# Optimization experiments

Measured on AMD Instinct MI355X. Metric: run time of the kernel, lower is better.

Reference implementation:

```python
import jax, jax.numpy as jnp
import numpy as np

B, N, D = 4, 2048, 1024
HEADS, DIM_HEAD = 16, 64
INNER = HEADS * DIM_HEAD  # 1024
SCALE = DIM_HEAD ** -0.5


def setup_inputs() -> dict:
    key = jax.random.key(0)
    ks = jax.random.split(key, 8)
    w = 0.02
    return {
        "x":  jax.random.normal(ks[0], (B, N, D), dtype=jnp.float32),
        "Wq": jax.random.normal(ks[1], (D, INNER), dtype=jnp.float32) * w,
        "bq": jax.random.normal(ks[2], (INNER,), dtype=jnp.float32) * w,
        "Wv": jax.random.normal(ks[3], (D, INNER), dtype=jnp.float32) * w,
        "bv": jax.random.normal(ks[4], (INNER,), dtype=jnp.float32) * w,
        "Wo": jax.random.normal(ks[5], (INNER, D), dtype=jnp.float32) * w,
        "bo": jax.random.normal(ks[6], (D,), dtype=jnp.float32) * w,
    }


def reference(x, Wq, bq, Wv, bv, Wo, bo):
    b, n, _ = x.shape
    q = x @ Wq + bq                      # [b, n, inner]
    v = x @ Wv + bv                      # [b, n, inner]
    # split heads -> [b, h, n, d]
    q = q.reshape(b, n, HEADS, DIM_HEAD).transpose(0, 2, 1, 3).astype(jnp.float32)
    v = v.reshape(b, n, HEADS, DIM_HEAD).transpose(0, 2, 1, 3)
    # k = q (self L2 attention)
    AB = jnp.einsum('bhid,bhjd->bhij', q, q)          # [b, h, n, n]
    AA = jnp.sum(q * q, axis=-1, keepdims=True)       # [b, h, n, 1]
    BB = jnp.swapaxes(AA, -1, -2)                     # [b, h, 1, n]
    sim = -(AA - 2.0 * AB + BB) * SCALE               # negative scaled L2 distance
    attn = jax.nn.softmax(sim, axis=-1)
    out = jnp.einsum('bhij,bhjd->bhid', attn, v)      # [b, h, n, d]
    out = out.transpose(0, 2, 1, 3).reshape(b, n, INNER)
    return out @ Wo + bo
```

## Files before the change

### kernel.cpp

```cpp
#include <hip/hip_runtime.h>
#include <hip/hip_bf16.h>

#define SEQ 2048
#define SCALE 0.125f
#define LOG2E 1.4426950408889634f
#define ALPHA 0.6005612049f

typedef __bf16 bf16;
typedef __bf16 bf16x4 __attribute__((ext_vector_type(4)));
typedef __bf16 bf16x8 __attribute__((ext_vector_type(8)));
typedef _Float16 f16;
typedef _Float16 f16x2 __attribute__((ext_vector_type(2)));
typedef _Float16 f16x4 __attribute__((ext_vector_type(4)));
typedef _Float16 f16x8 __attribute__((ext_vector_type(8)));
typedef float f32x4 __attribute__((ext_vector_type(4)));
typedef unsigned int u32;
typedef unsigned int u32x2 __attribute__((ext_vector_type(2)));
typedef unsigned int u32x4 __attribute__((ext_vector_type(4)));

__device__ __forceinline__ f16x2 pk_f16(float a, float b) {
    return __builtin_bit_cast(f16x2, __builtin_amdgcn_cvt_pkrtz(a, b));
}

__device__ __forceinline__ void gl_lds16(const void* g, void* l) {
    __builtin_amdgcn_global_load_lds((const __attribute__((address_space(1))) u32*)g,
                                     (__attribute__((address_space(3))) u32*)l, 16, 0, 0);
}


__global__ __launch_bounds__(256) void k_cast_x(const float4* __restrict__ x,
                                                bf16x4* __restrict__ xb) {
    int t = blockIdx.x * 256 + threadIdx.x;
    float4 f = x[t];
    bf16x4 o;
    o[0] = (bf16)f.x; o[1] = (bf16)f.y; o[2] = (bf16)f.z; o[3] = (bf16)f.w;
    xb[t] = o;
}

__global__ __launch_bounds__(256) void k_transpose_cast(const float* __restrict__ src,
                                                        bf16* __restrict__ dst) {
    __shared__ float tile[32][33];
    int bx = blockIdx.x * 32;
    int by = blockIdx.y * 32;
    int tx = threadIdx.x;
    int ty = threadIdx.y;
#pragma unroll
    for (int j = 0; j < 32; j += 8)
        tile[ty + j][tx] = src[(size_t)(by + ty + j) * 1024 + bx + tx];
    __syncthreads();
#pragma unroll
    for (int j = 0; j < 32; j += 8)
        dst[(size_t)(bx + ty + j) * 1024 + by + tx] = (bf16)tile[tx][ty + j];
}


__global__ __launch_bounds__(256) void k_gemm_qv(const bf16* __restrict__ Xb,
                                                 const bf16* __restrict__ Wqvt,
                                                 const float* __restrict__ bq,
                                                 const float* __restrict__ bv,
                                                 bf16* __restrict__ Q,
                                                 f16* __restrict__ Vt,
                                                 float* __restrict__ QN) {
    constexpr int K = 1024;
    __shared__ bf16 As[128 * 32];
    __shared__ bf16 Bs[128 * 32];
    int t = threadIdx.x, w = t >> 6, l = t & 63;
    int blockN = blockIdx.x * 128, blockM = blockIdx.y * 128;
    int wm = w & 1, wn = w >> 1;
    int lr = l & 15, quad = l >> 4, q8 = quad * 8;
    int skcol = (l & 3) * 8;
    bool isQ = blockN < 1024;

    f32x4 acc[4][4] = {};
    const bf16* Ab = Xb + (size_t)blockM * K;
    const bf16* Bb = Wqvt + (size_t)blockN * K;

    for (int k0 = 0; k0 < K; k0 += 32) {
#pragma unroll
        for (int c2 = 0; c2 < 2; ++c2) {
            int c = 2 * w + c2;
            int row = c * 16 + (l >> 2);
            gl_lds16(Ab + (size_t)row * K + k0 + skcol, As + c * 512);
            gl_lds16(Bb + (size_t)row * K + k0 + skcol, Bs + c * 512);
        }
        __syncthreads();
        const bf16* Aw = As + wm * 64 * 32;
        const bf16* Bw = Bs + wn * 64 * 32;
        bf16x8 af[4], bfr[4];
#pragma unroll
        for (int mi = 0; mi < 4; ++mi) af[mi] = *(const bf16x8*)(Aw + (mi * 16 + lr) * 32 + q8);
#pragma unroll
        for (int ni = 0; ni < 4; ++ni) bfr[ni] = *(const bf16x8*)(Bw + (ni * 16 + lr) * 32 + q8);
        if (isQ) {
#pragma unroll
            for (int mi = 0; mi < 4; ++mi)
#pragma unroll
                for (int ni = 0; ni < 4; ++ni)
                    acc[mi][ni] = __builtin_amdgcn_mfma_f32_16x16x32_bf16(af[mi], bfr[ni], acc[mi][ni], 0, 0, 0);
        } else {
#pragma unroll
            for (int mi = 0; mi < 4; ++mi)
#pragma unroll
                for (int ni = 0; ni < 4; ++ni)
                    acc[mi][ni] = __builtin_amdgcn_mfma_f32_16x16x32_bf16(bfr[ni], af[mi], acc[mi][ni], 0, 0, 0);
        }
        __syncthreads();
    }

    int colbase = blockN + wn * 64;
    if (isQ) {
        int h = colbase >> 6;
        float bias[4];
#pragma unroll
        for (int ni = 0; ni < 4; ++ni) bias[ni] = bq[colbase + ni * 16 + lr];
#pragma unroll
        for (int mi = 0; mi < 4; ++mi) {
#pragma unroll
            for (int r = 0; r < 4; ++r) {
                int m = blockM + wm * 64 + mi * 16 + quad * 4 + r;
                int b = m >> 11, s = m & 2047;
                int bh = (b << 4) + h;
                float qsq = 0.f;
#pragma unroll
                for (int ni = 0; ni < 4; ++ni) {
                    float v = (acc[mi][ni][r] + bias[ni]) * ALPHA;
                    bf16 vb = (bf16)v;
                    Q[((size_t)bh * SEQ + s) * 64 + ni * 16 + lr] = vb;
                    float vr = (float)vb;
                    qsq += vr * vr;
                }
                qsq += __shfl_xor(qsq, 1);
                qsq += __shfl_xor(qsq, 2);
                qsq += __shfl_xor(qsq, 4);
                qsq += __shfl_xor(qsq, 8);
                if (lr == 0) QN[(size_t)bh * SEQ + s] = -0.5f * qsq;
            }
        }
    } else {
        int h = (colbase - 1024) >> 6;
        int b = blockM >> 11;
        int bh = (b << 4) + h;
        int s_base = (blockM & 2047) + wm * 64;
        const float* bvh = bv + (colbase - 1024);
#pragma unroll
        for (int ni = 0; ni < 4; ++ni) {
#pragma unroll
            for (int r = 0; r < 4; ++r) {
                int dh = ni * 16 + quad * 4 + r;
                float bias = bvh[dh];
#pragma unroll
                for (int mi = 0; mi < 4; ++mi) {
                    int s = s_base + mi * 16 + lr;
                    Vt[((size_t)bh * 64 + dh) * SEQ + s] = (f16)(acc[mi][ni][r] + bias);
                }
            }
        }
    }
}


__global__ __launch_bounds__(256, 4) void k_attn(const bf16* __restrict__ Q,
                                                 const f16* __restrict__ Vt,
                                                 const float* __restrict__ QN,
                                                 bf16* __restrict__ AO) {
    __shared__ bf16 Ks[64 * 64];
    __shared__ f16 Vs[64 * 64];
    __shared__ float BBl[2048];

    int t = threadIdx.x, w = t >> 6, l = t & 63;
    int bh = blockIdx.y;
    int i0 = blockIdx.x * 128;
    const bf16* Qh = Q + (size_t)bh * SEQ * 64;
    const f16* Vh = Vt + (size_t)bh * 64 * SEQ;
    int lr = l & 15, quad = l >> 4, q8 = quad * 8, lr7 = lr & 7;

    {
        const float4* QN4 = (const float4*)(QN + (size_t)bh * SEQ);
        float4* BB4 = (float4*)BBl;
        BB4[t] = QN4[t];
        BB4[t + 256] = QN4[t + 256];
    }

    bf16x8 af[2][2];
#pragma unroll
    for (int mi = 0; mi < 2; ++mi)
#pragma unroll
        for (int kc = 0; kc < 2; ++kc)
            af[mi][kc] = *(const bf16x8*)(Qh + (size_t)(i0 + w * 32 + mi * 16 + lr) * 64 + kc * 32 + q8);

    f32x4 oacc[2][4] = {};
    f32x4 dacc[2] = {};
    const f16x4 ones = {(f16)1.f, (f16)1.f, (f16)1.f, (f16)1.f};

    int kb[2];
#pragma unroll
    for (int kc = 0; kc < 2; ++kc) kb[kc] = lr * 64 + (((kc * 4 + quad) ^ lr7) * 8);
    int voff[4];
#pragma unroll
    for (int di = 0; di < 4; ++di) voff[di] = (di * 16 + lr) * 64;
    int npo[2];
#pragma unroll
    for (int np = 0; np < 2; ++np) npo[np] = ((np * 4 + quad) ^ lr7) * 8;

    int sr0 = t >> 3, sc = t & 7;
    int sr1 = sr0 + 32;
    int ksl0 = sr0 * 64 + ((sc ^ (sr0 & 7)) * 8);
    int ksl1 = sr1 * 64 + ((sc ^ (sr1 & 7)) * 8);
    int np_s = sc >> 2, ni1_s = (sc >> 1) & 1, q0_s = (sc & 1) * 2;
    int cpA = np_s * 4 + q0_s, cpB = cpA + 1;
    int vdA0 = sr0 * 64 + ((cpA ^ (sr0 & 7)) * 8) + ni1_s * 4;
    int vdB0 = sr0 * 64 + ((cpB ^ (sr0 & 7)) * 8) + ni1_s * 4;
    int vdA1 = sr1 * 64 + ((cpA ^ (sr1 & 7)) * 8) + ni1_s * 4;
    int vdB1 = sr1 * 64 + ((cpB ^ (sr1 & 7)) * 8) + ni1_s * 4;

    u32x4 rk0 = *(const u32x4*)(Qh + (size_t)sr0 * 64 + sc * 8);
    u32x4 rk1 = *(const u32x4*)(Qh + (size_t)sr1 * 64 + sc * 8);
    u32x4 rv0 = *(const u32x4*)(Vh + (size_t)sr0 * SEQ + sc * 8);
    u32x4 rv1 = *(const u32x4*)(Vh + (size_t)sr1 * SEQ + sc * 8);

    for (int j0 = 0; j0 < SEQ; j0 += 64) {
        __syncthreads();
        *(u32x4*)(Ks + ksl0) = rk0;
        *(u32x4*)(Ks + ksl1) = rk1;
        {
            u32x2 lo0 = {rv0[0], rv0[1]}, hi0 = {rv0[2], rv0[3]};
            u32x2 lo1 = {rv1[0], rv1[1]}, hi1 = {rv1[2], rv1[3]};
            *(u32x2*)(Vs + vdA0) = lo0;
            *(u32x2*)(Vs + vdB0) = hi0;
            *(u32x2*)(Vs + vdA1) = lo1;
            *(u32x2*)(Vs + vdB1) = hi1;
        }
        int jn = j0 + 64;
        if (jn < SEQ) {
            rk0 = *(const u32x4*)(Qh + (size_t)(jn + sr0) * 64 + sc * 8);
            rk1 = *(const u32x4*)(Qh + (size_t)(jn + sr1) * 64 + sc * 8);
            rv0 = *(const u32x4*)(Vh + (size_t)sr0 * SEQ + jn + sc * 8);
            rv1 = *(const u32x4*)(Vh + (size_t)sr1 * SEQ + jn + sc * 8);
        }
        __syncthreads();

#pragma unroll
        for (int np = 0; np < 2; ++np) {
            f16x4 pf[2][2];
#pragma unroll
            for (int ni1 = 0; ni1 < 2; ++ni1) {
                int ni = np * 2 + ni1;
                bf16x8 bk0 = *(const bf16x8*)(Ks + ni * 1024 + kb[0]);
                bf16x8 bk1 = *(const bf16x8*)(Ks + ni * 1024 + kb[1]);
                f32x4 bbt = *(const f32x4*)(BBl + j0 + ni * 16 + quad * 4);
                f32x4 sT0 = bbt, sT1 = bbt;
                sT0 = __builtin_amdgcn_mfma_f32_16x16x32_bf16(bk0, af[0][0], sT0, 0, 0, 0);
                sT0 = __builtin_amdgcn_mfma_f32_16x16x32_bf16(bk1, af[0][1], sT0, 0, 0, 0);
                sT1 = __builtin_amdgcn_mfma_f32_16x16x32_bf16(bk0, af[1][0], sT1, 0, 0, 0);
                sT1 = __builtin_amdgcn_mfma_f32_16x16x32_bf16(bk1, af[1][1], sT1, 0, 0, 0);

                float p00 = __builtin_amdgcn_exp2f(sT0[0]);
                float p01 = __builtin_amdgcn_exp2f(sT0[1]);
                float p02 = __builtin_amdgcn_exp2f(sT0[2]);
                float p03 = __builtin_amdgcn_exp2f(sT0[3]);
                float p10 = __builtin_amdgcn_exp2f(sT1[0]);
                float p11 = __builtin_amdgcn_exp2f(sT1[1]);
                float p12 = __builtin_amdgcn_exp2f(sT1[2]);
                float p13 = __builtin_amdgcn_exp2f(sT1[3]);

                f16x2 a0 = pk_f16(p00, p01);
                f16x2 a1 = pk_f16(p02, p03);
                f16x2 b0 = pk_f16(p10, p11);
                f16x2 b1 = pk_f16(p12, p13);
                pf[0][ni1] = f16x4{a0[0], a0[1], a1[0], a1[1]};
                pf[1][ni1] = f16x4{b0[0], b0[1], b1[0], b1[1]};

                dacc[0] = __builtin_amdgcn_mfma_f32_16x16x16f16(pf[0][ni1], ones, dacc[0], 0, 0, 0);
                dacc[1] = __builtin_amdgcn_mfma_f32_16x16x16f16(pf[1][ni1], ones, dacc[1], 0, 0, 0);
            }
#pragma unroll
            for (int di = 0; di < 4; ++di) {
                f16x8 vf8 = *(const f16x8*)(Vs + voff[di] + npo[np]);
                f16x4 vlo = __builtin_shufflevector(vf8, vf8, 0, 1, 2, 3);
                f16x4 vhi = __builtin_shufflevector(vf8, vf8, 4, 5, 6, 7);
                oacc[0][di] = __builtin_amdgcn_mfma_f32_16x16x16f16(pf[0][0], vlo, oacc[0][di], 0, 0, 0);
                oacc[1][di] = __builtin_amdgcn_mfma_f32_16x16x16f16(pf[1][0], vlo, oacc[1][di], 0, 0, 0);
                oacc[0][di] = __builtin_amdgcn_mfma_f32_16x16x16f16(pf[0][1], vhi, oacc[0][di], 0, 0, 0);
                oacc[1][di] = __builtin_amdgcn_mfma_f32_16x16x16f16(pf[1][1], vhi, oacc[1][di], 0, 0, 0);
            }
        }
    }

    int b = bh >> 4, h = bh & 15;
#pragma unroll
    for (int mi = 0; mi < 2; ++mi) {
#pragma unroll
        for (int r = 0; r < 4; ++r) {
            float inv = 1.f / dacc[mi][r];
            int s = i0 + w * 32 + mi * 16 + quad * 4 + r;
#pragma unroll
            for (int di = 0; di < 4; ++di) {
                AO[((size_t)(b * SEQ + s)) * 1024 + h * 64 + di * 16 + lr] = (bf16)(oacc[mi][di][r] * inv);
            }
        }
    }
}


__global__ __launch_bounds__(256) void k_gemm_out(const bf16* __restrict__ AO,
                                                  const bf16* __restrict__ Wot,
                                                  const float* __restrict__ bo,
                                                  float* __restrict__ out) {
    constexpr int K = 1024;
    __shared__ bf16 As[128 * 32];
    __shared__ bf16 Bs[128 * 32];
    int t = threadIdx.x, w = t >> 6, l = t & 63;
    int blockN = blockIdx.x * 128, blockM = blockIdx.y * 128;
    int wm = w & 1, wn = w >> 1;
    int lr = l & 15, quad = l >> 4, q8 = quad * 8;
    int skcol = (l & 3) * 8;

    f32x4 acc[4][4] = {};
    const bf16* Ab = AO + (size_t)blockM * K;
    const bf16* Bb = Wot + (size_t)blockN * K;

    for (int k0 = 0; k0 < K; k0 += 32) {
#pragma unroll
        for (int c2 = 0; c2 < 2; ++c2) {
            int c = 2 * w + c2;
            int row = c * 16 + (l >> 2);
            gl_lds16(Ab + (size_t)row * K + k0 + skcol, As + c * 512);
            gl_lds16(Bb + (size_t)row * K + k0 + skcol, Bs + c * 512);
        }
        __syncthreads();
        const bf16* Aw = As + wm * 64 * 32;
        const bf16* Bw = Bs + wn * 64 * 32;
        bf16x8 af[4], bfr[4];
#pragma unroll
        for (int mi = 0; mi < 4; ++mi) af[mi] = *(const bf16x8*)(Aw + (mi * 16 + lr) * 32 + q8);
#pragma unroll
        for (int ni = 0; ni < 4; ++ni) bfr[ni] = *(const bf16x8*)(Bw + (ni * 16 + lr) * 32 + q8);
#pragma unroll
        for (int mi = 0; mi < 4; ++mi)
#pragma unroll
            for (int ni = 0; ni < 4; ++ni)
                acc[mi][ni] = __builtin_amdgcn_mfma_f32_16x16x32_bf16(af[mi], bfr[ni], acc[mi][ni], 0, 0, 0);
        __syncthreads();
    }

    int colbase = blockN + wn * 64;
    float bias[4];
#pragma unroll
    for (int ni = 0; ni < 4; ++ni) bias[ni] = bo[colbase + ni * 16 + lr];
#pragma unroll
    for (int mi = 0; mi < 4; ++mi) {
#pragma unroll
        for (int r = 0; r < 4; ++r) {
            int m = blockM + wm * 64 + mi * 16 + quad * 4 + r;
#pragma unroll
            for (int ni = 0; ni < 4; ++ni) {
                out[(size_t)m * 1024 + colbase + ni * 16 + lr] = acc[mi][ni][r] + bias[ni];
            }
        }
    }
}


extern "C" void kernel_launch(void* const* d_in, const int* in_sizes, int n_in,
                              void* d_out, int out_size, void* d_ws, size_t ws_size,
                              hipStream_t stream) {
    const float* x  = (const float*)d_in[0];
    const float* Wq = (const float*)d_in[1];
    const float* bq = (const float*)d_in[2];
    const float* Wv = (const float*)d_in[3];
    const float* bv = (const float*)d_in[4];
    const float* Wo = (const float*)d_in[5];
    const float* bo = (const float*)d_in[6];
    float* out = (float*)d_out;

    char* ws = (char*)d_ws;
    bf16* Xb   = (bf16*)ws;
    bf16* Wqvt = (bf16*)(ws + (size_t)(16 << 20));
    bf16* Wot  = (bf16*)(ws + (size_t)(20 << 20));
    bf16* Qb   = (bf16*)(ws + (size_t)(22 << 20));
    f16*  Vtb  = (f16*)(ws + (size_t)(38 << 20));
    float* QN  = (float*)(ws + (size_t)(54 << 20));
    bf16* AO   = Xb;

    k_cast_x<<<8192, 256, 0, stream>>>((const float4*)x, (bf16x4*)Xb);
    dim3 tb(32, 8);
    k_transpose_cast<<<dim3(32, 32), tb, 0, stream>>>(Wq, Wqvt);
    k_transpose_cast<<<dim3(32, 32), tb, 0, stream>>>(Wv, Wqvt + 1024 * 1024);
    k_transpose_cast<<<dim3(32, 32), tb, 0, stream>>>(Wo, Wot);
    k_gemm_qv<<<dim3(16, 64), 256, 0, stream>>>(Xb, Wqvt, bq, bv, Qb, Vtb, QN);
    k_attn<<<dim3(16, 64), 256, 0, stream>>>(Qb, Vtb, QN, AO);
    k_gemm_out<<<dim3(8, 64), 256, 0, stream>>>(AO, Wot, bo, out);
}
```

Baseline: 292.7 us.

## Use 16x16x32 f16 MFMA for PV via permlane swaps and plain V layout

Replaces the pairs of 16x16x16 f16 MFMAs for the P·V product and the row-sum with single 16x16x32 f16 MFMAs. The P fragments are rearranged across lanes with v_permlane32/16_swap so they match the K=32 operand layout. This lets V be stored to LDS with plain 16-byte swizzled writes instead of split 8-byte scatter writes. The cost is extra cross-lane permute instructions per tile, and correctness depends on the lane remapping matching the V layout.

```diff
diff --git a/kernel.cpp b/kernel.cpp
--- a/kernel.cpp
+++ b/kernel.cpp
@@ -20,6 +20,14 @@
 
 __device__ __forceinline__ f16x2 pk_f16(float a, float b) {
     return __builtin_bit_cast(f16x2, __builtin_amdgcn_cvt_pkrtz(a, b));
+}
+
+__device__ __forceinline__ u32 pk_u32(float a, float b) {
+    return __builtin_bit_cast(u32, __builtin_amdgcn_cvt_pkrtz(a, b));
+}
+
+__device__ __forceinline__ f32x4 mfma_f16_32(f16x8 a, f16x8 b, f32x4 c) {
+    return __builtin_amdgcn_mfma_f32_16x16x32_f16(a, b, c, 0, 0, 0);
 }
 
 __device__ __forceinline__ void gl_lds16(const void* g, void* l) {
@@ -190,7 +198,8 @@
 
     f32x4 oacc[2][4] = {};
     f32x4 dacc[2] = {};
-    const f16x4 ones = {(f16)1.f, (f16)1.f, (f16)1.f, (f16)1.f};
+    const f16x8 ones8 = {(f16)1.f, (f16)1.f, (f16)1.f, (f16)1.f,
+                         (f16)1.f, (f16)1.f, (f16)1.f, (f16)1.f};
 
     int kb[2];
 #pragma unroll
@@ -204,14 +213,8 @@
 
     int sr0 = t >> 3, sc = t & 7;
     int sr1 = sr0 + 32;
-    int ksl0 = sr0 * 64 + ((sc ^ (sr0 & 7)) * 8);
-    int ksl1 = sr1 * 64 + ((sc ^ (sr1 & 7)) * 8);
-    int np_s = sc >> 2, ni1_s = (sc >> 1) & 1, q0_s = (sc & 1) * 2;
-    int cpA = np_s * 4 + q0_s, cpB = cpA + 1;
-    int vdA0 = sr0 * 64 + ((cpA ^ (sr0 & 7)) * 8) + ni1_s * 4;
-    int vdB0 = sr0 * 64 + ((cpB ^ (sr0 & 7)) * 8) + ni1_s * 4;
-    int vdA1 = sr1 * 64 + ((cpA ^ (sr1 & 7)) * 8) + ni1_s * 4;
-    int vdB1 = sr1 * 64 + ((cpB ^ (sr1 & 7)) * 8) + ni1_s * 4;
+    int sl0 = sr0 * 64 + ((sc ^ (sr0 & 7)) * 8);
+    int sl1 = sr1 * 64 + ((sc ^ (sr1 & 7)) * 8);
 
     u32x4 rk0 = *(const u32x4*)(Qh + (size_t)sr0 * 64 + sc * 8);
     u32x4 rk1 = *(const u32x4*)(Qh + (size_t)sr1 * 64 + sc * 8);
@@ -220,16 +223,10 @@
 
     for (int j0 = 0; j0 < SEQ; j0 += 64) {
         __syncthreads();
-        *(u32x4*)(Ks + ksl0) = rk0;
-        *(u32x4*)(Ks + ksl1) = rk1;
-        {
-            u32x2 lo0 = {rv0[0], rv0[1]}, hi0 = {rv0[2], rv0[3]};
-            u32x2 lo1 = {rv1[0], rv1[1]}, hi1 = {rv1[2], rv1[3]};
-            *(u32x2*)(Vs + vdA0) = lo0;
-            *(u32x2*)(Vs + vdB0) = hi0;
-            *(u32x2*)(Vs + vdA1) = lo1;
-            *(u32x2*)(Vs + vdB1) = hi1;
-        }
+        *(u32x4*)(Ks + sl0) = rk0;
+        *(u32x4*)(Ks + sl1) = rk1;
+        *(u32x4*)(Vs + sl0) = rv0;
+        *(u32x4*)(Vs + sl1) = rv1;
         int jn = j0 + 64;
         if (jn < SEQ) {
             rk0 = *(const u32x4*)(Qh + (size_t)(jn + sr0) * 64 + sc * 8);
@@ -241,7 +238,7 @@
 
 #pragma unroll
         for (int np = 0; np < 2; ++np) {
-            f16x4 pf[2][2];
+            u32 hA[2][2], hB[2][2];
 #pragma unroll
             for (int ni1 = 0; ni1 < 2; ++ni1) {
                 int ni = np * 2 + ni1;
@@ -263,25 +260,39 @@
                 float p12 = __builtin_amdgcn_exp2f(sT1[2]);
                 float p13 = __builtin_amdgcn_exp2f(sT1[3]);
 
-                f16x2 a0 = pk_f16(p00, p01);
-                f16x2 a1 = pk_f16(p02, p03);
-                f16x2 b0 = pk_f16(p10, p11);
-                f16x2 b1 = pk_f16(p12, p13);
-                pf[0][ni1] = f16x4{a0[0], a0[1], a1[0], a1[1]};
-                pf[1][ni1] = f16x4{b0[0], b0[1], b1[0], b1[1]};
-
-                dacc[0] = __builtin_amdgcn_mfma_f32_16x16x16f16(pf[0][ni1], ones, dacc[0], 0, 0, 0);
-                dacc[1] = __builtin_amdgcn_mfma_f32_16x16x16f16(pf[1][ni1], ones, dacc[1], 0, 0, 0);
-            }
+                hA[ni1][0] = pk_u32(p00, p01);
+                hA[ni1][1] = pk_u32(p02, p03);
+                hB[ni1][0] = pk_u32(p10, p11);
+                hB[ni1][1] = pk_u32(p12, p13);
+            }
+            f16x8 F8[2];
+            {
+                u32 a0 = hA[0][0], b0 = hA[1][0], a1 = hA[0][1], b1 = hA[1][1];
+                asm("v_permlane32_swap_b32 %0, %1" : "+v"(a0), "+v"(b0));
+                asm("v_permlane16_swap_b32 %0, %1" : "+v"(a0), "+v"(b0));
+                asm("v_permlane32_swap_b32 %0, %1" : "+v"(a1), "+v"(b1));
+                asm("v_permlane16_swap_b32 %0, %1" : "+v"(a1), "+v"(b1));
+                u32x4 fu = {a0, a1, b0, b1};
+                F8[0] = __builtin_bit_cast(f16x8, fu);
+            }
+            {
+                u32 a0 = hB[0][0], b0 = hB[1][0], a1 = hB[0][1], b1 = hB[1][1];
+                asm("v_permlane32_swap_b32 %0, %1" : "+v"(a0), "+v"(b0));
+                asm("v_permlane16_swap_b32 %0, %1" : "+v"(a0), "+v"(b0));
+                asm("v_permlane32_swap_b32 %0, %1" : "+v"(a1), "+v"(b1));
+                asm("v_permlane16_swap_b32 %0, %1" : "+v"(a1), "+v"(b1));
+                u32x4 fu = {a0, a1, b0, b1};
+                F8[1] = __builtin_bit_cast(f16x8, fu);
+            }
+
+            dacc[0] = mfma_f16_32(F8[0], ones8, dacc[0]);
+            dacc[1] = mfma_f16_32(F8[1], ones8, dacc[1]);
+
 #pragma unroll
             for (int di = 0; di < 4; ++di) {
                 f16x8 vf8 = *(const f16x8*)(Vs + voff[di] + npo[np]);
-                f16x4 vlo = __builtin_shufflevector(vf8, vf8, 0, 1, 2, 3);
-                f16x4 vhi = __builtin_shufflevector(vf8, vf8, 4, 5, 6, 7);
-                oacc[0][di] = __builtin_amdgcn_mfma_f32_16x16x16f16(pf[0][0], vlo, oacc[0][di], 0, 0, 0);
-                oacc[1][di] = __builtin_amdgcn_mfma_f32_16x16x16f16(pf[1][0], vlo, oacc[1][di], 0, 0, 0);
-                oacc[0][di] = __builtin_amdgcn_mfma_f32_16x16x16f16(pf[0][1], vhi, oacc[0][di], 0, 0, 0);
-                oacc[1][di] = __builtin_amdgcn_mfma_f32_16x16x16f16(pf[1][1], vhi, oacc[1][di], 0, 0, 0);
+                oacc[0][di] = mfma_f16_32(F8[0], vf8, oacc[0][di]);
+                oacc[1][di] = mfma_f16_32(F8[1], vf8, oacc[1][di]);
             }
         }
     }
```

Measured after the change: 275.1 us. 1.06x faster.
